# Optimization experiments

Hardware: AMD Instinct MI355X
Metric: run time of the kernel (lower is better)

## Reference

```python
import jax, jax.numpy as jnp
import numpy as np

BSZ = 5
PROJ = 1000
DET = 513
IMG = 362
NPIX = IMG * IMG          # 131044
NNZ = 20_000_000


def setup_inputs() -> dict:
    key = jax.random.key(0)
    k1, k2, k3, k4 = jax.random.split(key, 4)
    filtered_sino = jax.random.normal(k1, (BSZ, PROJ, DET, 1), dtype=jnp.float32)
    sp_vals = jax.random.uniform(k2, (NNZ,), dtype=jnp.float32)
    sp_rows = jax.random.randint(k3, (NNZ,), 0, NPIX, dtype=jnp.int32)
    sp_cols = jax.random.randint(k4, (NNZ,), 0, PROJ * DET, dtype=jnp.int32)
    return {"filtered_sino": filtered_sino, "sp_vals": sp_vals,
            "sp_rows": sp_rows, "sp_cols": sp_cols}


def reference(filtered_sino, sp_vals, sp_rows, sp_cols):
    # Flatten each sinogram to [PROJ*DET] (row-major: proj then det, as tf.reshape).
    sino_flat = filtered_sino.reshape(BSZ, PROJ * DET)

    def back_project(s):  # s: [PROJ*DET] -> [NPIX]
        # sparse COO @ dense vector: out[row] += val * s[col]
        return jax.ops.segment_sum(sp_vals * s[sp_cols], sp_rows, num_segments=NPIX)

    rec = jax.vmap(back_project)(sino_flat)          # [BSZ, NPIX]
    # sens_image = back-projection of an all-ones sinogram
    sens = jax.ops.segment_sum(sp_vals, sp_rows, num_segments=NPIX)  # [NPIX]
    out = (rec / sens).reshape(BSZ, IMG, IMG, 1)
    return out
```

## Files before the change

kernel.cpp:

```cpp
#include <hip/hip_runtime.h>
#include <hip/hip_fp16.h>

#define BSZ  5
#define PROJ 1000
#define DET  513
#define IMG  362
#define NPIX (IMG * IMG)
#define SINO (PROJ * DET)
#define NNZ  20000000

#define NSHARD     4
#define SHARD_COLS (SINO / NSHARD)
#define RB_SHIFT   10
#define RB_PX      1024
#define NRBIN      128
#define NBIN       (NRBIN * NSHARD)

#define SCAT_BLOCKS  256
#define CHUNK        78128
#define TILE         8192
#define SCT_THREADS  1024

#define CAP        200
#define CELLS_PER_BIN (SCAT_BLOCKS * CAP)
#define OVF_CAP    65536

#define ACC_THREADS  512

#define FXSCALE 16384.0f
#define FXINV   (1.0f / 16384.0f)
#define FXB     262144
#define NTAG    0x1000000u

typedef int      i32x4 __attribute__((ext_vector_type(4)));
typedef float    f32x4 __attribute__((ext_vector_type(4)));
typedef unsigned u32x4 __attribute__((ext_vector_type(4)));

__device__ __forceinline__ unsigned lds_off(const void* p) {
    return (unsigned)(size_t)p;
}
__device__ __forceinline__ void ds_add_u64_nr(unsigned off, unsigned long long v) {
    asm volatile("ds_add_u64 %0, %1" :: "v"(off), "v"(v) : "memory");
}
__device__ __forceinline__ void lgkm_drain() {
    asm volatile("s_waitcnt lgkmcnt(0)" ::: "memory");
}

__device__ __forceinline__ int bin_of(int row, int col) {
    return ((row >> RB_SHIFT) << 2) | (col / SHARD_COLS);
}


__global__ __launch_bounds__(SCT_THREADS) void k_scatter(
        const float* __restrict__ sino, u32x4* __restrict__ sino_b,
        const float* __restrict__ vals, const int* __restrict__ rows,
        const int* __restrict__ cols,
        unsigned* __restrict__ recA, unsigned short* __restrict__ recB,
        unsigned* __restrict__ gcnt,
        unsigned long long* __restrict__ ovf, unsigned* __restrict__ ovf_n) {
    __shared__ unsigned cnt[NBIN];
    __shared__ unsigned toff[NBIN];
    __shared__ unsigned ebase[NBIN];
    __shared__ unsigned bs2[NBIN];
    __shared__ unsigned wsum[8];
    __shared__ unsigned long long sdata[TILE];
    const int t = threadIdx.x;
    const int lane = t & 63;

    {
        const int cbase = blockIdx.x * (SCT_THREADS * 2) + t * 2;
#pragma unroll
        for (int k = 0; k < 2; ++k) {
            const int c = cbase + k;
            if (c < SINO) {
                unsigned b[5];
#pragma unroll
                for (int j = 0; j < 5; ++j) {
                    const unsigned u = __float_as_uint(sino[(size_t)j * SINO + c]);
                    b[j] = (u + 0x7FFFu + ((u >> 16) & 1u)) >> 16;
                }
                u32x4 o;
                o.x = b[0] | (b[1] << 16);
                o.y = b[2] | (b[3] << 16);
                o.z = b[4];
                o.w = 0u;
                sino_b[c] = o;
            }
        }
    }

    const int lo = blockIdx.x * CHUNK;
    const int hi = (lo + CHUNK < NNZ) ? lo + CHUNK : NNZ;
    if (lo >= hi) return;

    if (t < NBIN) {
        bs2[t] = ((unsigned)t * SCAT_BLOCKS + (unsigned)blockIdx.x) * CAP;
        cnt[t] = 0u;
    }

    i32x4 sr0, sr1, sq0, sq1; f32x4 sv0, sv1;
    {
        const int n0 = (lo + TILE < hi) ? TILE : (hi - lo);
        if (t * 8 < n0) {
            const int i4 = (lo + t * 8) >> 2;
            sr0 = __builtin_nontemporal_load(((const i32x4*)rows) + i4);
            sr1 = __builtin_nontemporal_load(((const i32x4*)rows) + i4 + 1);
            sq0 = __builtin_nontemporal_load(((const i32x4*)cols) + i4);
            sq1 = __builtin_nontemporal_load(((const i32x4*)cols) + i4 + 1);
            sv0 = __builtin_nontemporal_load(((const f32x4*)vals) + i4);
            sv1 = __builtin_nontemporal_load(((const f32x4*)vals) + i4 + 1);
        }
    }
    __syncthreads();

    for (int tb = lo; tb < hi; tb += TILE) {
        const int n = (tb + TILE < hi) ? TILE : (hi - tb);
        const bool act = (t * 8) < n;

        const i32x4 cr0 = sr0, cr1 = sr1, cq0 = sq0, cq1 = sq1;
        const f32x4 cv0 = sv0, cv1 = sv1;

        const int ntb = tb + TILE;
        if (ntb < hi) {
            const int nn = (ntb + TILE < hi) ? TILE : (hi - ntb);
            if (t * 8 < nn) {
                const int i4 = (ntb + t * 8) >> 2;
                sr0 = __builtin_nontemporal_load(((const i32x4*)rows) + i4);
                sr1 = __builtin_nontemporal_load(((const i32x4*)rows) + i4 + 1);
                sq0 = __builtin_nontemporal_load(((const i32x4*)cols) + i4);
                sq1 = __builtin_nontemporal_load(((const i32x4*)cols) + i4 + 1);
                sv0 = __builtin_nontemporal_load(((const f32x4*)vals) + i4);
                sv1 = __builtin_nontemporal_load(((const f32x4*)vals) + i4 + 1);
            }
        }

        unsigned long long r8[8];
        unsigned sl[8];
        if (act) {
#pragma unroll
            for (int k = 0; k < 8; ++k) {
                const int rr = (k < 4) ? cr0[k] : cr1[k - 4];
                const int qq = (k < 4) ? cq0[k] : cq1[k - 4];
                const float vf = (k < 4) ? cv0[k] : cv1[k - 4];
                const unsigned bn = (unsigned)bin_of(rr, qq);
                const unsigned vh = (unsigned)__half_as_ushort(__float2half(vf));
                r8[k] = ((unsigned long long)bn << 55)
                      | ((unsigned long long)(unsigned)(rr & (RB_PX - 1)) << 45)
                      | ((unsigned long long)(unsigned)qq << 26)
                      | (unsigned long long)vh;
                sl[k] = atomicAdd(&cnt[bn], 1u);
            }
        }
        __syncthreads();

        unsigned x = 0u, incl = 0u;
        if (t < NBIN) {
            x = cnt[t];
            incl = x;
#pragma unroll
            for (int o = 1; o < 64; o <<= 1) {
                const unsigned y = __shfl_up(incl, (unsigned)o, 64);
                if (lane >= o) incl += y;
            }
            if (lane == 63) wsum[t >> 6] = incl;
        }
        __syncthreads();
        if (t < NBIN) {
            unsigned wo = 0u;
            const int w = t >> 6;
            for (int k = 0; k < w; ++k) wo += wsum[k];
            const unsigned e = wo + incl - x;
            toff[t] = e;
            ebase[t] = bs2[t] - e;
            bs2[t] += x;
            cnt[t] = 0u;
        }
        __syncthreads();

        if (act) {
#pragma unroll
            for (int k = 0; k < 8; ++k) {
                const unsigned bn = (unsigned)(r8[k] >> 55);
                sdata[toff[bn] + sl[k]] = r8[k];
            }
        }
        __syncthreads();

        for (int j = t; j < n; j += SCT_THREADS) {
            const unsigned long long u = sdata[j];
            const unsigned sb = (unsigned)(u >> 55);
            const unsigned pos = ebase[sb] + (unsigned)j;
            const unsigned cb = (sb * SCAT_BLOCKS + (unsigned)blockIdx.x) * CAP;
            const unsigned pk = (unsigned)((u >> 26) & 0x1FFFFFFFu);
            const unsigned short vh = (unsigned short)(u & 0xFFFFu);
            if (pos - cb < CAP) {
                recA[pos] = pk;
                recB[pos] = vh;
            } else {
                const unsigned g = atomicAdd(ovf_n, 1u);
                if (g < OVF_CAP) ovf[g] = u;
            }
        }
        __syncthreads();
    }

    if (t < NBIN) {
        const unsigned cb = ((unsigned)t * SCAT_BLOCKS + (unsigned)blockIdx.x) * CAP;
        const unsigned total = bs2[t] - cb;
        gcnt[(size_t)blockIdx.x * NBIN + t] = (total < CAP) ? total : CAP;
    }
}

__global__ __launch_bounds__(ACC_THREADS) void k_accum(
        const unsigned* __restrict__ recA, const unsigned short* __restrict__ recB,
        const unsigned* __restrict__ gcnt, const u32x4* __restrict__ sino_b,
        const unsigned long long* __restrict__ ovf, const unsigned* __restrict__ ovf_n,
        float* __restrict__ acc) {
    __shared__ unsigned long long l8[RB_PX * 3];
    __shared__ unsigned fcnt[SCAT_BLOCKS];
    const int t = threadIdx.x;
    const int bin = blockIdx.x;
    for (int j = t; j < RB_PX * 3; j += ACC_THREADS) l8[j] = 0ull;
    if (t < SCAT_BLOCKS) fcnt[t] = gcnt[(size_t)t * NBIN + bin];
    __syncthreads();

    const unsigned binbase = (unsigned)bin * CELLS_PER_BIN;
    for (unsigned i = (unsigned)t; i < CELLS_PER_BIN; i += ACC_THREADS) {
        const unsigned frag = i / CAP;
        const unsigned slot = i - frag * CAP;
        const unsigned a = recA[binbase + i];
        const unsigned short hraw = recB[binbase + i];
        if (slot < fcnt[frag]) {
            const float v = __half2float(__ushort_as_half(hraw));
            const int col = (int)(a & 0x7FFFFu);
            const int lr  = (int)(a >> 19);
            const u32x4 sv = sino_b[col];
            const int q0 = __float2int_rn(v * __uint_as_float(sv.x << 16)         * FXSCALE);
            const int q1 = __float2int_rn(v * __uint_as_float(sv.x & 0xFFFF0000u) * FXSCALE);
            const int q2 = __float2int_rn(v * __uint_as_float(sv.y << 16)         * FXSCALE);
            const int q3 = __float2int_rn(v * __uint_as_float(sv.y & 0xFFFF0000u) * FXSCALE);
            const int q4 = __float2int_rn(v * __uint_as_float(sv.z << 16)         * FXSCALE);
            const int q5 = __float2int_rn(v * FXSCALE);
            const unsigned b = lds_off(&l8[(unsigned)lr * 3u]);
            ds_add_u64_nr(b,
                ((unsigned long long)(unsigned)q1 << 32) | (unsigned)(q0 + FXB));
            ds_add_u64_nr(b + 8,
                ((unsigned long long)(unsigned)q3 << 32) | (unsigned)(q2 + FXB));
            ds_add_u64_nr(b + 16,
                ((unsigned long long)((unsigned)q5 + NTAG) << 32) | (unsigned)(q4 + FXB));
        }
    }

    {
        unsigned n = *ovf_n;
        if (n > OVF_CAP) n = OVF_CAP;
        for (unsigned i = (unsigned)t; i < n; i += ACC_THREADS) {
            const unsigned long long u = ovf[i];
            if ((unsigned)(u >> 55) != (unsigned)bin) continue;
            const float v = __half2float(__ushort_as_half((unsigned short)(u & 0xFFFFu)));
            const unsigned pk = (unsigned)((u >> 26) & 0x1FFFFFFFu);
            const int col = (int)(pk & 0x7FFFFu);
            const int lr  = (int)(pk >> 19);
            const u32x4 sv = sino_b[col];
            const int q0 = __float2int_rn(v * __uint_as_float(sv.x << 16)         * FXSCALE);
            const int q1 = __float2int_rn(v * __uint_as_float(sv.x & 0xFFFF0000u) * FXSCALE);
            const int q2 = __float2int_rn(v * __uint_as_float(sv.y << 16)         * FXSCALE);
            const int q3 = __float2int_rn(v * __uint_as_float(sv.y & 0xFFFF0000u) * FXSCALE);
            const int q4 = __float2int_rn(v * __uint_as_float(sv.z << 16)         * FXSCALE);
            const int q5 = __float2int_rn(v * FXSCALE);
            const unsigned b = lds_off(&l8[(unsigned)lr * 3u]);
            ds_add_u64_nr(b,
                ((unsigned long long)(unsigned)q1 << 32) | (unsigned)(q0 + FXB));
            ds_add_u64_nr(b + 8,
                ((unsigned long long)(unsigned)q3 << 32) | (unsigned)(q2 + FXB));
            ds_add_u64_nr(b + 16,
                ((unsigned long long)((unsigned)q5 + NTAG) << 32) | (unsigned)(q4 + FXB));
        }
    }
    lgkm_drain();
    __syncthreads();

    float* dst = acc + (size_t)bin * (RB_PX * 6);
    for (int px = t; px < RB_PX; px += ACC_THREADS) {
        const unsigned long long a0 = l8[px * 3 + 0];
        const unsigned long long a1 = l8[px * 3 + 1];
        const unsigned long long a2 = l8[px * 3 + 2];
        const unsigned hi3 = (unsigned)(a2 >> 32);
        const unsigned n = hi3 >> 24;
        const long long nb = (long long)n * FXB;
        float* d = dst + px * 6;
        d[0] = (float)((long long)(unsigned)(a0 & 0xFFFFFFFFull) - nb) * FXINV;
        d[1] = (float)((int)(a0 >> 32)) * FXINV;
        d[2] = (float)((long long)(unsigned)(a1 & 0xFFFFFFFFull) - nb) * FXINV;
        d[3] = (float)((int)(a1 >> 32)) * FXINV;
        d[4] = (float)((long long)(unsigned)(a2 & 0xFFFFFFFFull) - nb) * FXINV;
        d[5] = (float)(hi3 & 0xFFFFFFu) * FXINV;
    }
}

__global__ void k_reduce(const float* __restrict__ acc, float* __restrict__ out) {
    const int p = blockIdx.x * blockDim.x + threadIdx.x;
    if (p < NPIX) {
        const int rbin = p >> RB_SHIFT, lr = p & (RB_PX - 1);
        float n0 = 0.f, n1 = 0.f, n2 = 0.f, n3 = 0.f, n4 = 0.f, den = 0.f;
#pragma unroll
        for (int s = 0; s < NSHARD; ++s) {
            const float* b = acc + ((size_t)(rbin * NSHARD + s) * RB_PX + lr) * 6;
            n0 += b[0]; n1 += b[1]; n2 += b[2];
            n3 += b[3]; n4 += b[4]; den += b[5];
        }
        const float inv = 1.f / den;
        out[0 * (size_t)NPIX + p] = n0 * inv;
        out[1 * (size_t)NPIX + p] = n1 * inv;
        out[2 * (size_t)NPIX + p] = n2 * inv;
        out[3 * (size_t)NPIX + p] = n3 * inv;
        out[4 * (size_t)NPIX + p] = n4 * inv;
    }
}


__global__ void bp_scatter_fb_kernel(const float* __restrict__ sino,
                                     const float* __restrict__ vals,
                                     const int*   __restrict__ rows,
                                     const int*   __restrict__ cols,
                                     float* __restrict__ acc) {
    const long long stride = (long long)gridDim.x * blockDim.x;
    for (long long i = (long long)blockIdx.x * blockDim.x + threadIdx.x;
         i < NNZ; i += stride) {
        const float v = vals[i];
        const int   r = rows[i];
        const int   c = cols[i];
        atomicAdd(acc + (size_t)BSZ * NPIX + r, v);
#pragma unroll
        for (int b = 0; b < BSZ; ++b)
            atomicAdd(acc + (size_t)b * NPIX + r, v * sino[(size_t)b * SINO + c]);
    }
}

__global__ void bp_divide_fb_kernel(const float* __restrict__ acc,
                                    float* __restrict__ out) {
    const int i = blockIdx.x * blockDim.x + threadIdx.x;
    if (i < BSZ * NPIX) {
        const int p = i % NPIX;
        out[i] = acc[i] / acc[(size_t)BSZ * NPIX + p];
    }
}


extern "C" void kernel_launch(void* const* d_in, const int* in_sizes, int n_in,
                              void* d_out, int out_size, void* d_ws, size_t ws_size,
                              hipStream_t stream) {
    const float* sino = (const float*)d_in[0];
    const float* vals = (const float*)d_in[1];
    const int*   rows = (const int*)d_in[2];
    const int*   cols = (const int*)d_in[3];
    float* out = (float*)d_out;

    const size_t recA_b   = (size_t)NBIN * CELLS_PER_BIN * 4;
    const size_t recB_b   = (size_t)NBIN * CELLS_PER_BIN * 2;
    const size_t sino_b_b = (size_t)SINO * 16;
    const size_t acc_b    = (size_t)NBIN * RB_PX * 6 * 4;
    const size_t gcnt_b   = (size_t)SCAT_BLOCKS * NBIN * 4;
    const size_t ovf_b    = (size_t)OVF_CAP * 8;
    const size_t need = recA_b + recB_b + sino_b_b + acc_b + gcnt_b + ovf_b + 16;

    if (ws_size >= need) {
        char* w = (char*)d_ws;
        unsigned*       recA = (unsigned*)w;                w += recA_b;
        unsigned short* recB = (unsigned short*)w;          w += recB_b;
        u32x4*    sinob  = (u32x4*)w;                       w += sino_b_b;
        float*    acc    = (float*)w;                       w += acc_b;
        unsigned* gcnt   = (unsigned*)w;                    w += gcnt_b;
        unsigned long long* ovf = (unsigned long long*)w;   w += ovf_b;
        unsigned* ovf_n  = (unsigned*)w;

        (void)hipMemsetAsync(ovf_n, 0, 4, stream);
        k_scatter<<<SCAT_BLOCKS, SCT_THREADS, 0, stream>>>(
            sino, sinob, vals, rows, cols, recA, recB, gcnt, ovf, ovf_n);
        k_accum<<<NBIN, ACC_THREADS, 0, stream>>>(
            recA, recB, gcnt, sinob, ovf, ovf_n, acc);
        k_reduce<<<(NPIX + 255) / 256, 256, 0, stream>>>(acc, out);
    } else {
        float* acc = (float*)d_ws;
        (void)hipMemsetAsync(acc, 0, (size_t)(BSZ + 1) * NPIX * sizeof(float), stream);
        bp_scatter_fb_kernel<<<2048, 256, 0, stream>>>(sino, vals, rows, cols, acc);
        bp_divide_fb_kernel<<<(BSZ * NPIX + 255) / 256, 256, 0, stream>>>(acc, out);
    }
}
```

Before: 225.2 us.

## Replace tiled LDS counting-sort scatter with direct atomic-slot global writes

```diff
diff --git a/kernel.cpp b/kernel.cpp
--- a/kernel.cpp
+++ b/kernel.cpp
@@ -18,7 +18,6 @@
 
 #define SCAT_BLOCKS  256
 #define CHUNK        78128
-#define TILE         8192
 #define SCT_THREADS  1024
 
 #define CAP        200
@@ -59,13 +58,7 @@
         unsigned* __restrict__ gcnt,
         unsigned long long* __restrict__ ovf, unsigned* __restrict__ ovf_n) {
     __shared__ unsigned cnt[NBIN];
-    __shared__ unsigned toff[NBIN];
-    __shared__ unsigned ebase[NBIN];
-    __shared__ unsigned bs2[NBIN];
-    __shared__ unsigned wsum[8];
-    __shared__ unsigned long long sdata[TILE];
     const int t = threadIdx.x;
-    const int lane = t & 63;
 
     {
         const int cbase = blockIdx.x * (SCT_THREADS * 2) + t * 2;
@@ -89,124 +82,43 @@
         }
     }
 
+    if (t < NBIN) cnt[t] = 0u;
+    __syncthreads();
+
     const int lo = blockIdx.x * CHUNK;
     const int hi = (lo + CHUNK < NNZ) ? lo + CHUNK : NNZ;
-    if (lo >= hi) return;
-
-    if (t < NBIN) {
-        bs2[t] = ((unsigned)t * SCAT_BLOCKS + (unsigned)blockIdx.x) * CAP;
-        cnt[t] = 0u;
-    }
-
-    i32x4 sr0, sr1, sq0, sq1; f32x4 sv0, sv1;
-    {
-        const int n0 = (lo + TILE < hi) ? TILE : (hi - lo);
-        if (t * 8 < n0) {
-            const int i4 = (lo + t * 8) >> 2;
-            sr0 = __builtin_nontemporal_load(((const i32x4*)rows) + i4);
-            sr1 = __builtin_nontemporal_load(((const i32x4*)rows) + i4 + 1);
-            sq0 = __builtin_nontemporal_load(((const i32x4*)cols) + i4);
-            sq1 = __builtin_nontemporal_load(((const i32x4*)cols) + i4 + 1);
-            sv0 = __builtin_nontemporal_load(((const f32x4*)vals) + i4);
-            sv1 = __builtin_nontemporal_load(((const f32x4*)vals) + i4 + 1);
-        }
-    }
-    __syncthreads();
-
-    for (int tb = lo; tb < hi; tb += TILE) {
-        const int n = (tb + TILE < hi) ? TILE : (hi - tb);
-        const bool act = (t * 8) < n;
-
-        const i32x4 cr0 = sr0, cr1 = sr1, cq0 = sq0, cq1 = sq1;
-        const f32x4 cv0 = sv0, cv1 = sv1;
-
-        const int ntb = tb + TILE;
-        if (ntb < hi) {
-            const int nn = (ntb + TILE < hi) ? TILE : (hi - ntb);
-            if (t * 8 < nn) {
-                const int i4 = (ntb + t * 8) >> 2;
-                sr0 = __builtin_nontemporal_load(((const i32x4*)rows) + i4);
-                sr1 = __builtin_nontemporal_load(((const i32x4*)rows) + i4 + 1);
-                sq0 = __builtin_nontemporal_load(((const i32x4*)cols) + i4);
-                sq1 = __builtin_nontemporal_load(((const i32x4*)cols) + i4 + 1);
-                sv0 = __builtin_nontemporal_load(((const f32x4*)vals) + i4);
-                sv1 = __builtin_nontemporal_load(((const f32x4*)vals) + i4 + 1);
-            }
-        }
-
-        unsigned long long r8[8];
-        unsigned sl[8];
-        if (act) {
-#pragma unroll
-            for (int k = 0; k < 8; ++k) {
-                const int rr = (k < 4) ? cr0[k] : cr1[k - 4];
-                const int qq = (k < 4) ? cq0[k] : cq1[k - 4];
-                const float vf = (k < 4) ? cv0[k] : cv1[k - 4];
-                const unsigned bn = (unsigned)bin_of(rr, qq);
-                const unsigned vh = (unsigned)__half_as_ushort(__float2half(vf));
-                r8[k] = ((unsigned long long)bn << 55)
-                      | ((unsigned long long)(unsigned)(rr & (RB_PX - 1)) << 45)
-                      | ((unsigned long long)(unsigned)qq << 26)
-                      | (unsigned long long)vh;
-                sl[k] = atomicAdd(&cnt[bn], 1u);
-            }
-        }
-        __syncthreads();
-
-        unsigned x = 0u, incl = 0u;
-        if (t < NBIN) {
-            x = cnt[t];
-            incl = x;
-#pragma unroll
-            for (int o = 1; o < 64; o <<= 1) {
-                const unsigned y = __shfl_up(incl, (unsigned)o, 64);
-                if (lane >= o) incl += y;
-            }
-            if (lane == 63) wsum[t >> 6] = incl;
-        }
-        __syncthreads();
-        if (t < NBIN) {
-            unsigned wo = 0u;
-            const int w = t >> 6;
-            for (int k = 0; k < w; ++k) wo += wsum[k];
-            const unsigned e = wo + incl - x;
-            toff[t] = e;
-            ebase[t] = bs2[t] - e;
-            bs2[t] += x;
-            cnt[t] = 0u;
-        }
-        __syncthreads();
-
-        if (act) {
-#pragma unroll
-            for (int k = 0; k < 8; ++k) {
-                const unsigned bn = (unsigned)(r8[k] >> 55);
-                sdata[toff[bn] + sl[k]] = r8[k];
-            }
-        }
-        __syncthreads();
-
-        for (int j = t; j < n; j += SCT_THREADS) {
-            const unsigned long long u = sdata[j];
-            const unsigned sb = (unsigned)(u >> 55);
-            const unsigned pos = ebase[sb] + (unsigned)j;
-            const unsigned cb = (sb * SCAT_BLOCKS + (unsigned)blockIdx.x) * CAP;
-            const unsigned pk = (unsigned)((u >> 26) & 0x1FFFFFFFu);
-            const unsigned short vh = (unsigned short)(u & 0xFFFFu);
-            if (pos - cb < CAP) {
+    const unsigned blkoff = (unsigned)blockIdx.x * CAP;
+
+    for (int i4 = lo / 4 + t; i4 * 4 < hi; i4 += SCT_THREADS) {
+        const i32x4 r = __builtin_nontemporal_load(((const i32x4*)rows) + i4);
+        const i32x4 q = __builtin_nontemporal_load(((const i32x4*)cols) + i4);
+        const f32x4 v = __builtin_nontemporal_load(((const f32x4*)vals) + i4);
+#pragma unroll
+        for (int k = 0; k < 4; ++k) {
+            const int rr = r[k];
+            const int qq = q[k];
+            const float vf = v[k];
+            const unsigned bn = (unsigned)bin_of(rr, qq);
+            const unsigned pk = ((unsigned)(rr & (RB_PX - 1)) << 19) | (unsigned)qq;
+            const unsigned vh = (unsigned)__half_as_ushort(__float2half(vf));
+            const unsigned slot = atomicAdd(&cnt[bn], 1u);
+            if (slot < CAP) {
+                const unsigned pos = bn * (SCAT_BLOCKS * CAP) + blkoff + slot;
                 recA[pos] = pk;
-                recB[pos] = vh;
+                recB[pos] = (unsigned short)vh;
             } else {
                 const unsigned g = atomicAdd(ovf_n, 1u);
-                if (g < OVF_CAP) ovf[g] = u;
+                if (g < OVF_CAP)
+                    ovf[g] = ((unsigned long long)bn << 55)
+                           | ((unsigned long long)pk << 26)
+                           | (unsigned long long)vh;
             }
         }
-        __syncthreads();
-    }
+    }
+    __syncthreads();
 
     if (t < NBIN) {
-        const unsigned cb = ((unsigned)t * SCAT_BLOCKS + (unsigned)blockIdx.x) * CAP;
-        const unsigned total = bs2[t] - cb;
+        const unsigned total = cnt[t];
         gcnt[(size_t)blockIdx.x * NBIN + t] = (total < CAP) ? total : CAP;
     }
 }
```

Result: slower. 651.1 us (+189.1%).
